# Optimization experiments

Hardware: AMD Instinct MI355X
Metric: run time of the kernel (lower is better)

The kernel has to match this reference:

```python
import jax, jax.numpy as jnp
import numpy as np

VOCAB = 333
D_MODEL = 333
N_HEADS = 8
D_HEAD = 64
INNER = N_HEADS * D_HEAD  # 512
MAX_LEN = 333
B, S = 64, 333


def setup_inputs() -> dict:
    key = jax.random.key(0)
    ks = jax.random.split(key, 9)
    sc_in = (1.0 / np.sqrt(D_MODEL)).astype(np.float32)
    sc_inner = (1.0 / np.sqrt(INNER)).astype(np.float32)
    return {
        "xs": jax.random.randint(ks[0], (B, S), 0, VOCAB),
        "emb": jax.random.normal(ks[1], (VOCAB, D_MODEL), dtype=jnp.float32),
        "Wq": jax.random.normal(ks[2], (D_MODEL, INNER), dtype=jnp.float32) * sc_in,
        "bq": jnp.zeros((INNER,), dtype=jnp.float32),
        "Wk": jax.random.normal(ks[3], (D_MODEL, INNER), dtype=jnp.float32) * sc_in,
        "bk": jnp.zeros((INNER,), dtype=jnp.float32),
        "Wv": jax.random.normal(ks[4], (D_MODEL, INNER), dtype=jnp.float32) * sc_in,
        "bv": jnp.zeros((INNER,), dtype=jnp.float32),
        "Er": jax.random.normal(ks[5], (MAX_LEN, D_HEAD), dtype=jnp.float32) * 0.02,
        "Wo": jax.random.normal(ks[6], (INNER, D_MODEL), dtype=jnp.float32) * sc_inner,
        "bo": jnp.zeros((D_MODEL,), dtype=jnp.float32),
    }


def _skew(qe):
    # Music Transformer skew trick: qe [B,H,S,L] (L==S) -> Srel [B,H,S,S]
    b, h, s, l = qe.shape
    padded = jnp.pad(qe, ((0, 0), (0, 0), (0, 0), (1, 0)))  # [B,H,S,L+1]
    return padded.reshape(b, h, l + 1, s)[:, :, 1:, :]       # [B,H,S,S]


def reference(xs, emb, Wq, bq, Wk, bk, Wv, bv, Er, Wo, bo):
    x = emb[xs]  # [B,S,D]
    b, s, _ = x.shape

    def heads(w, bias):
        return (x @ w + bias).reshape(b, s, N_HEADS, D_HEAD).transpose(0, 2, 1, 3)

    q = heads(Wq, bq)  # [B,H,S,Dh]
    k = heads(Wk, bk)
    v = heads(Wv, bv)

    er = Er[MAX_LEN - s:]                                   # [S,Dh]
    qk = jnp.einsum("bhsd,bhtd->bhst", q, k)               # content scores
    srel = _skew(jnp.einsum("bhsd,ld->bhsl", q, er))       # relative scores
    scores = (qk + srel) / np.sqrt(D_HEAD).astype(np.float32)

    causal = jnp.tril(jnp.ones((s, s), dtype=bool))         # predictive mask
    scores = jnp.where(causal, scores, jnp.float32(-1e9))
    attn = jax.nn.softmax(scores, axis=-1)

    out = jnp.einsum("bhst,bhtd->bhsd", attn, v)            # [B,H,S,Dh]
    out = out.transpose(0, 2, 1, 3).reshape(b, s, INNER)
    return out @ Wo + bo                                    # [B,S,D]
```

## Files before the change

### kernel.cpp

```cpp
#include <hip/hip_runtime.h>
#include <hip/hip_bf16.h>

#define BB 64
#define SS 333
#define NH 8
#define DH 64
#define NI 512
#define DM 333
#define M1 21312
#define KP 384
#define NQ 1536
#define RS1 1536

typedef __attribute__((ext_vector_type(8))) short short8v;
typedef __attribute__((ext_vector_type(4))) float f32x4;

__device__ inline short f2bf(float f) {
    unsigned u = __float_as_uint(f);
    u += 0x7fffu + ((u >> 16) & 1u);
    return (short)(u >> 16);
}

__device__ __forceinline__ void gload16(const void* g, void* l) {
    __builtin_amdgcn_global_load_lds(
        (const __attribute__((address_space(1))) void*)g,
        (__attribute__((address_space(3))) void*)l, 16, 0, 0);
}

#define CN0 (SS * DH)
#define CN1 (DM * KP)
#define CN2 (NQ * KP)
#define CN3 (384 * NI)
#define CNT (CN0 + CN1 + CN2 + CN3)

__global__ __launch_bounds__(256) void conv_all_kernel(
    const float* __restrict__ Er, const float* __restrict__ emb,
    const float* __restrict__ Wq, const float* __restrict__ Wk,
    const float* __restrict__ Wv, const float* __restrict__ Wo,
    short* __restrict__ eb, short* __restrict__ embb,
    short* __restrict__ wt, short* __restrict__ wot)
{
    int i = blockIdx.x * 256 + threadIdx.x;
    if (i < CN0) {
        eb[i] = f2bf(Er[i]);
        return;
    }
    i -= CN0;
    if (i < CN1) {
        int v = i / KP, k = i - v * KP;
        embb[i] = (k < DM) ? f2bf(emb[(size_t)v * DM + k]) : (short)0;
        return;
    }
    i -= CN1;
    if (i < CN2) {
        int n = i / KP, k = i - n * KP;
        int mat = n >> 9, c = n & 511;
        const float* W = (mat == 0) ? Wq : (mat == 1) ? Wk : Wv;
        wt[i] = (k < DM) ? f2bf(W[(size_t)k * NI + c]) : (short)0;
        return;
    }
    i -= CN2;
    if (i < CN3) {
        int n = i >> 9, k = i & 511;
        wot[i] = (n < DM) ? f2bf(Wo[(size_t)k * DM + n]) : (short)0;
    }
}

__global__ __launch_bounds__(256) void yqkv_kernel(
    const short* __restrict__ embb, const short* __restrict__ wt,
    const float* __restrict__ bq, const float* __restrict__ bk, const float* __restrict__ bv,
    short* __restrict__ Y)
{
    __shared__ __align__(16) short abuf[2][128 * 64];
    __shared__ __align__(16) short bbuf[2][128 * 64];

    const int row0 = blockIdx.x * 128;
    const int n0   = blockIdx.y * 128;
    const int t = threadIdx.x;
    const int lane = t & 63, w = t >> 6;
    const int l15 = lane & 15, lq = lane >> 4;
    const int wr = w >> 1, wc = w & 1;

    f32x4 acc[4][4];
#pragma unroll
    for (int mi = 0; mi < 4; ++mi)
#pragma unroll
        for (int nj = 0; nj < 4; ++nj) { f32x4 z = {0.f,0.f,0.f,0.f}; acc[mi][nj] = z; }

    auto stage = [&](int buf, int k0) {
#pragma unroll
        for (int i = 0; i < 4; ++i) {
            int idx = (w * 4 + i) * 64 + lane;
            int row = idx >> 3, sp = idx & 7;
            int ar = row0 + row; ar = ar < DM ? ar : DM - 1;
            gload16(embb + (size_t)ar * KP + k0 + ((sp ^ (row & 7)) << 3),
                    &abuf[buf][(w * 4 + i) * 512]);
        }
#pragma unroll
        for (int i = 0; i < 4; ++i) {
            int idx = (w * 4 + i) * 64 + lane;
            int row = idx >> 3, sp = idx & 7;
            gload16(wt + (size_t)(n0 + row) * KP + k0 + ((sp ^ (row & 7)) << 3),
                    &bbuf[buf][(w * 4 + i) * 512]);
        }
    };

    stage(0, 0);
    __syncthreads();
    for (int tk = 0; tk < 6; ++tk) {
        if (tk < 5) stage((tk + 1) & 1, (tk + 1) * 64);
        const short* ab = abuf[tk & 1];
        const short* bb = bbuf[tk & 1];
#pragma unroll
        for (int kh = 0; kh < 2; ++kh) {
            short8v af[4], bfv[4];
#pragma unroll
            for (int mi = 0; mi < 4; ++mi) {
                int row = wr * 64 + mi * 16 + l15;
                int sp = (lq + 4 * kh) ^ (row & 7);
                af[mi] = *(const short8v*)(ab + row * 64 + sp * 8);
            }
#pragma unroll
            for (int nj = 0; nj < 4; ++nj) {
                int row = wc * 64 + nj * 16 + l15;
                int sp = (lq + 4 * kh) ^ (row & 7);
                bfv[nj] = *(const short8v*)(bb + row * 64 + sp * 8);
            }
            __builtin_amdgcn_s_setprio(1);
#pragma unroll
            for (int mi = 0; mi < 4; ++mi)
#pragma unroll
                for (int nj = 0; nj < 4; ++nj)
                    acc[mi][nj] = __builtin_amdgcn_mfma_f32_16x16x32_bf16(af[mi], bfv[nj], acc[mi][nj], 0, 0, 0);
            __builtin_amdgcn_s_setprio(0);
        }
        __syncthreads();
    }

    const int mat = n0 >> 9;
    const float* bias = (mat == 0) ? bq : (mat == 1) ? bk : bv;
    const int cb = (n0 & 511) + wc * 64;
#pragma unroll
    for (int nj = 0; nj < 4; ++nj) {
        float bvv = bias[cb + nj * 16 + l15];
        int colg = n0 + wc * 64 + nj * 16 + l15;
#pragma unroll
        for (int mi = 0; mi < 4; ++mi)
#pragma unroll
            for (int r = 0; r < 4; ++r) {
                int rowg = row0 + wr * 64 + mi * 16 + lq * 4 + r;
                Y[(size_t)rowg * NQ + colg] = f2bf(acc[mi][nj][r] + bvv);
            }
    }
}

__global__ __launch_bounds__(512) __attribute__((amdgpu_waves_per_eu(4, 4)))
void attn_mfma_kernel(
    const short* __restrict__ Y, const int* __restrict__ xs,
    const short* __restrict__ eb, short* __restrict__ attnb)
{
    __shared__ __align__(16) short k_lds[64 * 64];
    __shared__ __align__(16) short vT_lds[64 * 64];
    __shared__ __align__(16) short vrow[64 * 64];
    __shared__ __align__(16) short p_lds[128 * 64];
    __shared__ int tok_lds[SS];

    const int p = blockIdx.x;
    const int h = p & 7;
    const int rem = p >> 3;
    const int pi = rem % 3;
    const int b = rem / 3;
    const int t = threadIdx.x;
    const int lane = t & 63, w = t >> 6;
    const int l15 = lane & 15, lq = lane >> 4;

    if (t < SS) tok_lds[t] = xs[b * SS + t];
    __syncthreads();

    const int thi = 5 - pi;
    const int tlo = pi;
    const int tt = w >> 2;
    const int sw = w & 3;
    const int ti = tt ? tlo : thi;
    const int iw = ti * 64 + 16 * sw;

    const short* Yh = Y + h * 64;

    int qr = iw + l15; if (qr > SS - 1) qr = SS - 1;
    const short* qrow = Yh + (size_t)tok_lds[qr] * RS1;
    const short8v qa0 = *(const short8v*)(qrow + lq * 8);
    const short8v qa1 = *(const short8v*)(qrow + 32 + lq * 8);

    float l4[4];
    f32x4 o[4];
#pragma unroll
    for (int r = 0; r < 4; ++r) { l4[r] = 0.f; }
#pragma unroll
    for (int nd = 0; nd < 4; ++nd) { f32x4 z = {0.f, 0.f, 0.f, 0.f}; o[nd] = z; }

    asm volatile("s_waitcnt vmcnt(0)" ::: "memory");

    const int maxjs = thi;
    for (int js = 0; js <= maxjs; ++js) {
        const int j0 = js * 64;
        __syncthreads();
        {
            int row = t >> 3, sp = t & 7;
            int jg = j0 + row; if (jg > SS - 1) jg = SS - 1;
            gload16(Yh + (size_t)tok_lds[jg] * RS1 + 1024 + ((sp ^ (row & 7)) << 3),
                    &vrow[(size_t)(t & 448) * 8]);
        }
        {
            int row = t >> 3, sp = t & 7;
            int jg = j0 + row; if (jg > SS - 1) jg = SS - 1;
            gload16(Yh + (size_t)tok_lds[jg] * RS1 + 512 + ((sp ^ (row & 7)) << 3),
                    &k_lds[(size_t)(t & 448) * 8]);
        }
        asm volatile("s_waitcnt vmcnt(1)" ::: "memory");
        {
            const int kc = w;
            const int d = lane;
            short8v vv;
#pragma unroll
            for (int j = 0; j < 8; ++j)
                vv[j] = vrow[(kc * 8 + j) * 64 + (((d >> 3) ^ j) << 3) + (d & 7)];
            *(short8v*)(vT_lds + (size_t)d * 64 + ((kc ^ (d & 7)) << 3)) = vv;
        }
        __syncthreads();

        if (tt == 0 || js <= tlo) {
            f32x4 sc[4];
            __builtin_amdgcn_s_setprio(1);
#pragma unroll
            for (int n = 0; n < 4; ++n) {
                int row = n * 16 + l15;
                short8v k0 = *(const short8v*)((char*)k_lds + ((row * 128 + lq * 16) ^ ((row & 7) << 4)));
                short8v k1 = *(const short8v*)((char*)k_lds + ((row * 128 + 64 + lq * 16) ^ ((row & 7) << 4)));
                f32x4 z = {0.f, 0.f, 0.f, 0.f};
                z = __builtin_amdgcn_mfma_f32_16x16x32_bf16(qa0, k0, z, 0, 0, 0);
                sc[n] = __builtin_amdgcn_mfma_f32_16x16x32_bf16(qa1, k1, z, 0, 0, 0);
            }
            __builtin_amdgcn_s_setprio(0);

            const int sbA = SS - 16 - iw + j0;
            auto qepair = [&](int n2) -> f32x4 {
                int lg = sbA + n2 * 16 + l15;
                lg = lg < 0 ? 0 : (lg > SS - 1 ? SS - 1 : lg);
                const short* er = eb + (size_t)lg * DH;
                short8v e0 = *(const short8v*)(er + lq * 8);
                short8v e1 = *(const short8v*)(er + 32 + lq * 8);
                f32x4 z = {0.f, 0.f, 0.f, 0.f};
                z = __builtin_amdgcn_mfma_f32_16x16x32_bf16(qa0, e0, z, 0, 0, 0);
                return __builtin_amdgcn_mfma_f32_16x16x32_bf16(qa1, e1, z, 0, 0, 0);
            };
            short* pw = p_lds + w * 1024;
            f32x4 qprev = qepair(0);
#pragma unroll
            for (int n = 0; n < 4; ++n) {
                f32x4 qcur = qepair(n + 1);
                float psum[4];
#pragma unroll
                for (int r = 0; r < 4; ++r) {
                    int irel = lq * 4 + r;
                    int u = 15 - irel + l15;
                    int srcl = (lane & 48) | (u & 15);
                    float elo = __shfl(qprev[r], srcl);
                    float ehi = __shfl(qcur[r], srcl);
                    float srel = (u < 16) ? elo : ehi;
                    int jrel = n * 16 + l15;
                    bool ok = (j0 + jrel) <= (iw + irel);
                    float sv = ok ? (sc[n][r] + srel) * 0.125f - 16.0f : -1e9f;
                    float pv = __expf(sv);
                    psum[r] = pv;
                    *(short*)((char*)pw + ((irel * 128 + jrel * 2) ^ ((irel & 7) << 4))) = f2bf(pv);
                }
#pragma unroll
                for (int r = 0; r < 4; ++r)
                    l4[r] += psum[r];
                qprev = qcur;
            }

            __builtin_amdgcn_s_setprio(1);
#pragma unroll
            for (int kb2 = 0; kb2 < 2; ++kb2) {
                short8v pa = *(const short8v*)((char*)pw + ((l15 * 128 + kb2 * 64 + lq * 16) ^ ((l15 & 7) << 4)));
#pragma unroll
                for (int nd = 0; nd < 4; ++nd) {
                    int d = nd * 16 + l15;
                    short8v vf = *(const short8v*)((char*)vT_lds + ((size_t)d * 128 + (((kb2 * 4 + lq) ^ (d & 7)) << 4)));
                    o[nd] = __builtin_amdgcn_mfma_f32_16x16x32_bf16(pa, vf, o[nd], 0, 0, 0);
                }
            }
            __builtin_amdgcn_s_setprio(0);
        }
    }

#pragma unroll
    for (int r = 0; r < 4; ++r) {
        float ls = l4[r];
        ls += __shfl_xor(ls, 1);
        ls += __shfl_xor(ls, 2);
        ls += __shfl_xor(ls, 4);
        ls += __shfl_xor(ls, 8);
        int i = iw + lq * 4 + r;
        if (i < SS) {
            float rl = 1.0f / ls;
#pragma unroll
            for (int nd = 0; nd < 4; ++nd)
                attnb[(size_t)(b * SS + i) * NI + h * 64 + nd * 16 + l15] = f2bf(o[nd][r] * rl);
        }
    }
}

__global__ __launch_bounds__(256) void oproj_mfma_kernel(
    const short* __restrict__ ab_g, const short* __restrict__ wot,
    const float* __restrict__ bo, float* __restrict__ out)
{
    __shared__ __align__(16) short abuf[2][128 * 64];
    __shared__ __align__(16) short bbuf[2][128 * 64];

    const int row0 = blockIdx.x * 128;
    const int n0   = blockIdx.y * 128;
    const int t = threadIdx.x;
    const int lane = t & 63, w = t >> 6;
    const int l15 = lane & 15, lq = lane >> 4;
    const int wr = w >> 1, wc = w & 1;

    f32x4 acc[4][4];
#pragma unroll
    for (int mi = 0; mi < 4; ++mi)
#pragma unroll
        for (int nj = 0; nj < 4; ++nj) { f32x4 z = {0.f,0.f,0.f,0.f}; acc[mi][nj] = z; }

    auto stage = [&](int buf, int k0) {
#pragma unroll
        for (int i = 0; i < 4; ++i) {
            int idx = (w * 4 + i) * 64 + lane;
            int row = idx >> 3, sp = idx & 7;
            int rg = row0 + row; rg = rg < M1 ? rg : M1 - 1;
            gload16(ab_g + (size_t)rg * NI + k0 + ((sp ^ (row & 7)) << 3),
                    &abuf[buf][(w * 4 + i) * 512]);
        }
#pragma unroll
        for (int i = 0; i < 4; ++i) {
            int idx = (w * 4 + i) * 64 + lane;
            int row = idx >> 3, sp = idx & 7;
            gload16(wot + (size_t)(n0 + row) * NI + k0 + ((sp ^ (row & 7)) << 3),
                    &bbuf[buf][(w * 4 + i) * 512]);
        }
    };

    stage(0, 0);
    __syncthreads();
    for (int tk = 0; tk < 8; ++tk) {
        if (tk < 7) stage((tk + 1) & 1, (tk + 1) * 64);
        const short* ab = abuf[tk & 1];
        const short* bb = bbuf[tk & 1];
#pragma unroll
        for (int kh = 0; kh < 2; ++kh) {
            short8v af[4], bfv[4];
#pragma unroll
            for (int mi = 0; mi < 4; ++mi) {
                int row = wr * 64 + mi * 16 + l15;
                int sp = (lq + 4 * kh) ^ (row & 7);
                af[mi] = *(const short8v*)(ab + row * 64 + sp * 8);
            }
#pragma unroll
            for (int nj = 0; nj < 4; ++nj) {
                int row = wc * 64 + nj * 16 + l15;
                int sp = (lq + 4 * kh) ^ (row & 7);
                bfv[nj] = *(const short8v*)(bb + row * 64 + sp * 8);
            }
            __builtin_amdgcn_s_setprio(1);
#pragma unroll
            for (int mi = 0; mi < 4; ++mi)
#pragma unroll
                for (int nj = 0; nj < 4; ++nj)
                    acc[mi][nj] = __builtin_amdgcn_mfma_f32_16x16x32_bf16(af[mi], bfv[nj], acc[mi][nj], 0, 0, 0);
            __builtin_amdgcn_s_setprio(0);
        }
        __syncthreads();
    }

#pragma unroll
    for (int nj = 0; nj < 4; ++nj) {
        int colg = n0 + wc * 64 + nj * 16 + l15;
        float bvv = (colg < DM) ? bo[colg] : 0.f;
#pragma unroll
        for (int mi = 0; mi < 4; ++mi)
#pragma unroll
            for (int r = 0; r < 4; ++r) {
                int rowg = row0 + wr * 64 + mi * 16 + lq * 4 + r;
                if (rowg < M1 && colg < DM)
                    out[(size_t)rowg * DM + colg] = acc[mi][nj][r] + bvv;
            }
    }
}

extern "C" void kernel_launch(void* const* d_in, const int* in_sizes, int n_in,
                              void* d_out, int out_size, void* d_ws, size_t ws_size,
                              hipStream_t stream) {
    const int*   xs  = (const int*)d_in[0];
    const float* emb = (const float*)d_in[1];
    const float* Wq  = (const float*)d_in[2];
    const float* bq  = (const float*)d_in[3];
    const float* Wk  = (const float*)d_in[4];
    const float* bk  = (const float*)d_in[5];
    const float* Wv  = (const float*)d_in[6];
    const float* bv  = (const float*)d_in[7];
    const float* Er  = (const float*)d_in[8];
    const float* Wo  = (const float*)d_in[9];
    const float* bo  = (const float*)d_in[10];
    float* out = (float*)d_out;

    short* attnb = (short*)d_ws;
    short* Y    = attnb + (size_t)M1 * NI;
    short* embb = Y + (size_t)384 * NQ;
    short* wt   = embb + (size_t)DM * KP;
    short* wot  = wt + (size_t)NQ * KP;
    short* eb   = wot + (size_t)384 * NI;

    conv_all_kernel<<<(CNT + 255) / 256, 256, 0, stream>>>(Er, emb, Wq, Wk, Wv, Wo,
                                                           eb, embb, wt, wot);
    dim3 g1(3, 12);
    yqkv_kernel<<<g1, 256, 0, stream>>>(embb, wt, bq, bk, bv, Y);
    attn_mfma_kernel<<<BB * NH * 3, 512, 0, stream>>>(Y, xs, eb, attnb);
    dim3 g3((M1 + 127) / 128, 3);
    oproj_mfma_kernel<<<g3, 256, 0, stream>>>(attnb, wot, bo, out);
}
```

Before: 111.8 us.

## Precompute per-token relative-position scores in a table instead of per-tile MFMA

Queries depend only on the token id, so the q·Er relative scores take only vocab × length × heads distinct values. A new kernel precomputes that table once, already scaled and shifted, and the attention kernel gathers from it. This removes the per-tile Er MFMAs, the global Er loads and the skew shuffles. In exchange it adds a kernel launch and scattered fp32 gathers from a table of about 3.5 MB that must stay cache-resident.

```diff
diff --git a/kernel.cpp b/kernel.cpp
--- a/kernel.cpp
+++ b/kernel.cpp
@@ -11,6 +11,7 @@
 #define KP 384
 #define NQ 1536
 #define RS1 1536
+#define VT2 110889
 
 typedef __attribute__((ext_vector_type(8))) short short8v;
 typedef __attribute__((ext_vector_type(4))) float f32x4;
@@ -154,10 +155,86 @@
     }
 }
 
+__global__ __launch_bounds__(256) void qet_kernel(
+    const short* __restrict__ Y, const short* __restrict__ eb,
+    float* __restrict__ QEt)
+{
+    __shared__ __align__(16) short abuf[128 * 64];
+    __shared__ __align__(16) short bbuf[128 * 64];
+
+    const int row0 = blockIdx.x * 128;
+    const int n0   = blockIdx.y * 128;
+    const int h    = blockIdx.z;
+    const int t = threadIdx.x;
+    const int lane = t & 63, w = t >> 6;
+    const int l15 = lane & 15, lq = lane >> 4;
+    const int wr = w >> 1, wc = w & 1;
+
+#pragma unroll
+    for (int i = 0; i < 4; ++i) {
+        int idx = (w * 4 + i) * 64 + lane;
+        int row = idx >> 3, sp = idx & 7;
+        int ar = row0 + row; ar = ar < DM ? ar : DM - 1;
+        gload16(Y + (size_t)ar * RS1 + h * 64 + ((sp ^ (row & 7)) << 3),
+                &abuf[(w * 4 + i) * 512]);
+    }
+#pragma unroll
+    for (int i = 0; i < 4; ++i) {
+        int idx = (w * 4 + i) * 64 + lane;
+        int row = idx >> 3, sp = idx & 7;
+        int br = n0 + row; br = br < SS ? br : SS - 1;
+        gload16(eb + (size_t)br * DH + ((sp ^ (row & 7)) << 3),
+                &bbuf[(w * 4 + i) * 512]);
+    }
+    __syncthreads();
+
+    f32x4 acc[4][4];
+#pragma unroll
+    for (int mi = 0; mi < 4; ++mi)
+#pragma unroll
+        for (int nj = 0; nj < 4; ++nj) { f32x4 z = {0.f,0.f,0.f,0.f}; acc[mi][nj] = z; }
+
+#pragma unroll
+    for (int kh = 0; kh < 2; ++kh) {
+        short8v af[4], bfv[4];
+#pragma unroll
+        for (int mi = 0; mi < 4; ++mi) {
+            int row = wr * 64 + mi * 16 + l15;
+            int sp = (lq + 4 * kh) ^ (row & 7);
+            af[mi] = *(const short8v*)(abuf + row * 64 + sp * 8);
+        }
+#pragma unroll
+        for (int nj = 0; nj < 4; ++nj) {
+            int row = wc * 64 + nj * 16 + l15;
+            int sp = (lq + 4 * kh) ^ (row & 7);
+            bfv[nj] = *(const short8v*)(bbuf + row * 64 + sp * 8);
+        }
+#pragma unroll
+        for (int mi = 0; mi < 4; ++mi)
+#pragma unroll
+            for (int nj = 0; nj < 4; ++nj)
+                acc[mi][nj] = __builtin_amdgcn_mfma_f32_16x16x32_bf16(af[mi], bfv[nj], acc[mi][nj], 0, 0, 0);
+    }
+
+    float* Qh = QEt + (size_t)h * VT2;
+#pragma unroll
+    for (int nj = 0; nj < 4; ++nj) {
+        int colg = n0 + wc * 64 + nj * 16 + l15;
+#pragma unroll
+        for (int mi = 0; mi < 4; ++mi)
+#pragma unroll
+            for (int r = 0; r < 4; ++r) {
+                int rowg = row0 + wr * 64 + mi * 16 + lq * 4 + r;
+                if (rowg < SS && colg < SS)
+                    Qh[(size_t)rowg * SS + colg] = acc[mi][nj][r] * 0.125f - 16.0f;
+            }
+    }
+}
+
 __global__ __launch_bounds__(512) __attribute__((amdgpu_waves_per_eu(4, 4)))
 void attn_mfma_kernel(
     const short* __restrict__ Y, const int* __restrict__ xs,
-    const short* __restrict__ eb, short* __restrict__ attnb)
+    const float* __restrict__ QEt, short* __restrict__ attnb)
 {
     __shared__ __align__(16) short k_lds[64 * 64];
     __shared__ __align__(16) short vT_lds[64 * 64];
@@ -185,11 +262,19 @@
     const int iw = ti * 64 + 16 * sw;
 
     const short* Yh = Y + h * 64;
+    const float* QEh = QEt + (size_t)h * VT2;
 
     int qr = iw + l15; if (qr > SS - 1) qr = SS - 1;
     const short* qrow = Yh + (size_t)tok_lds[qr] * RS1;
     const short8v qa0 = *(const short8v*)(qrow + lq * 8);
     const short8v qa1 = *(const short8v*)(qrow + 32 + lq * 8);
+
+    int irow[4];
+#pragma unroll
+    for (int r = 0; r < 4; ++r) {
+        int i_ = iw + lq * 4 + r; if (i_ > SS - 1) i_ = SS - 1;
+        irow[r] = tok_lds[i_] * SS;
+    }
 
     float l4[4];
     f32x4 o[4];
@@ -242,42 +327,25 @@
             }
             __builtin_amdgcn_s_setprio(0);
 
-            const int sbA = SS - 16 - iw + j0;
-            auto qepair = [&](int n2) -> f32x4 {
-                int lg = sbA + n2 * 16 + l15;
-                lg = lg < 0 ? 0 : (lg > SS - 1 ? SS - 1 : lg);
-                const short* er = eb + (size_t)lg * DH;
-                short8v e0 = *(const short8v*)(er + lq * 8);
-                short8v e1 = *(const short8v*)(er + 32 + lq * 8);
-                f32x4 z = {0.f, 0.f, 0.f, 0.f};
-                z = __builtin_amdgcn_mfma_f32_16x16x32_bf16(qa0, e0, z, 0, 0, 0);
-                return __builtin_amdgcn_mfma_f32_16x16x32_bf16(qa1, e1, z, 0, 0, 0);
-            };
             short* pw = p_lds + w * 1024;
-            f32x4 qprev = qepair(0);
 #pragma unroll
             for (int n = 0; n < 4; ++n) {
-                f32x4 qcur = qepair(n + 1);
                 float psum[4];
 #pragma unroll
                 for (int r = 0; r < 4; ++r) {
                     int irel = lq * 4 + r;
-                    int u = 15 - irel + l15;
-                    int srcl = (lane & 48) | (u & 15);
-                    float elo = __shfl(qprev[r], srcl);
-                    float ehi = __shfl(qcur[r], srcl);
-                    float srel = (u < 16) ? elo : ehi;
+                    int li = (SS - 1) - (iw + irel) + j0 + n * 16 + l15;
+                    li = li < 0 ? 0 : (li > SS - 1 ? SS - 1 : li);
+                    float qet = QEh[irow[r] + li];
                     int jrel = n * 16 + l15;
                     bool ok = (j0 + jrel) <= (iw + irel);
-                    float sv = ok ? (sc[n][r] + srel) * 0.125f - 16.0f : -1e9f;
-                    float pv = __expf(sv);
+                    float pv = ok ? __expf(sc[n][r] * 0.125f + qet) : 0.f;
                     psum[r] = pv;
                     *(short*)((char*)pw + ((irel * 128 + jrel * 2) ^ ((irel & 7) << 4))) = f2bf(pv);
                 }
 #pragma unroll
                 for (int r = 0; r < 4; ++r)
                     l4[r] += psum[r];
-                qprev = qcur;
             }
 
             __builtin_amdgcn_s_setprio(1);
@@ -419,12 +487,15 @@
     short* wt   = embb + (size_t)DM * KP;
     short* wot  = wt + (size_t)NQ * KP;
     short* eb   = wot + (size_t)384 * NI;
+    float* QEt  = (float*)(eb + (size_t)SS * DH);
 
     conv_all_kernel<<<(CNT + 255) / 256, 256, 0, stream>>>(Er, emb, Wq, Wk, Wv, Wo,
                                                            eb, embb, wt, wot);
     dim3 g1(3, 12);
     yqkv_kernel<<<g1, 256, 0, stream>>>(embb, wt, bq, bk, bv, Y);
-    attn_mfma_kernel<<<BB * NH * 3, 512, 0, stream>>>(Y, xs, eb, attnb);
+    dim3 g2(3, 3, 8);
+    qet_kernel<<<g2, 256, 0, stream>>>(Y, eb, QEt);
+    attn_mfma_kernel<<<BB * NH * 3, 512, 0, stream>>>(Y, xs, QEt, attnb);
     dim3 g3((M1 + 127) / 128, 3);
     oproj_mfma_kernel<<<g3, 256, 0, stream>>>(attnb, wot, bo, out);
 }
```

Result: no change. 112.8 us (+0.8%).
